# Optimization experiments

Hardware: AMD Instinct MI355X
Metric: run time of the kernel (lower is better)

## Reference

```python
import jax, jax.numpy as jnp
import numpy as np

N_NODES = 50000
N_EDGES = 800000
FEAT = 64
HID = 128
N_TYPES = 4
N_REL = 3
N_LAYERS = 2
LN_EPS = 1e-5


def setup_inputs() -> dict:
    key = jax.random.key(0)
    ks = jax.random.split(key, 20)
    inp = {
        "z": jax.random.randint(ks[0], (N_NODES,), 0, 100, dtype=jnp.int32),
        "node_type": jax.random.randint(ks[1], (N_NODES,), 0, N_TYPES, dtype=jnp.int32),
        "edge_index": jax.random.randint(ks[2], (2, N_EDGES), 0, N_NODES, dtype=jnp.int32),
        "edge_type": jax.random.randint(ks[3], (N_EDGES,), 0, N_REL, dtype=jnp.int32),
        # learned parameters
        "z_embed": jax.random.normal(ks[4], (100, FEAT), jnp.float32),
        "enc_w1": jax.random.normal(ks[5], (N_TYPES, FEAT, HID), jnp.float32) * 0.05,
        "enc_b1": jnp.zeros((N_TYPES, HID), jnp.float32),
        "enc_w2": jax.random.normal(ks[6], (N_TYPES, HID, HID), jnp.float32) * 0.05,
        "enc_b2": jnp.zeros((N_TYPES, HID), jnp.float32),
        "lin_w": jax.random.normal(ks[7], (N_LAYERS, HID, HID), jnp.float32) * 0.05,
        "lin_b": jnp.zeros((N_LAYERS, HID), jnp.float32),
        "rel_w": jax.random.normal(ks[8], (N_LAYERS, N_REL, HID, HID), jnp.float32) * 0.05,
        "ln_g": jnp.ones((N_LAYERS, HID), jnp.float32),
        "ln_b": jnp.zeros((N_LAYERS, HID), jnp.float32),
        "reg_w": jax.random.normal(ks[9], (HID, 1), jnp.float32) * 0.05,
        "reg_b": jnp.zeros((1,), jnp.float32),
    }
    return inp


def _layer_norm(x, g, b):
    mu = jnp.mean(x, axis=-1, keepdims=True)
    var = jnp.mean((x - mu) ** 2, axis=-1, keepdims=True)
    return (x - mu) * jax.lax.rsqrt(var + LN_EPS) * g + b


def reference(z, node_type, edge_index, edge_type, z_embed, enc_w1, enc_b1,
              enc_w2, enc_b2, lin_w, lin_b, rel_w, ln_g, ln_b, reg_w, reg_b):
    n = z.shape[0]
    # FeatureBuilder (site_ads=None path): atomic-number embedding lookup
    raw = z_embed[z]  # [N, FEAT]
    # TypeSpecificEncoder: run all 4 type MLPs, select per node by node_type
    h = jax.nn.relu(jnp.einsum('nd,tdh->nth', raw, enc_w1) + enc_b1)  # [N,T,H]
    enc_all = jnp.einsum('nth,tho->nto', h, enc_w2) + enc_b2           # [N,T,H]
    x = jnp.take_along_axis(enc_all, node_type[:, None, None].astype(jnp.int32), axis=1)[:, 0, :]

    src, dst = edge_index[0], edge_index[1]
    deg = jax.ops.segment_sum(jnp.ones((edge_type.shape[0],), x.dtype), dst, num_segments=n)
    deg = jnp.clip(deg, 1.0, None)[:, None]  # [N,1]

    for l in range(N_LAYERS):
        out = jnp.zeros_like(x)
        x_src = x[src]  # [E, H] gathered source features
        for r in range(N_REL):
            mask = (edge_type == r).astype(x.dtype)[:, None]
            msg = (x_src * mask) @ rel_w[l, r]  # [E, H]
            out = out + jax.ops.segment_sum(msg, dst, num_segments=n)
        out = out / deg
        x = _layer_norm(x @ lin_w[l] + lin_b[l] + out, ln_g[l], ln_b[l])

    pooled = jnp.mean(x, axis=0)  # mean pooling, mask = all ones
    return pooled @ reg_w + reg_b  # [1]
```

## Files before the change

kernel.cpp:

```cpp
#include <hip/hip_runtime.h>

#define N_NODES 50000
#define N_EDGES 800000
#define FEAT 64
#define HID 128
#define N_TYPES 4
#define N_REL 3
#define N_LAYERS 2
#define LN_EPS 1e-5f
#define NROWS 50016
#define NG32 1563
#define CAP 64
#define NBKT 196
#define CAP1 4608
#define EPB 4096
#define BINCAP 56
#define NCOMBO 400
#define WT_STRIDE 136

typedef __attribute__((ext_vector_type(8))) short bf16x8;
typedef __attribute__((ext_vector_type(16))) float f32x16;
typedef __attribute__((ext_vector_type(2))) float f32x2;

static __device__ inline unsigned short f2bf(float f) {
    unsigned int u = __float_as_uint(f);
    return (unsigned short)((u + 0x7fffu + ((u >> 16) & 1u)) >> 16);
}
static __device__ inline unsigned int packbf2(float lo, float hi) {
    return (unsigned int)f2bf(lo) | ((unsigned int)f2bf(hi) << 16);
}

static __device__ inline void acc8_fp8(float* a, uint2 w) {
    f32x2 d0 = __builtin_amdgcn_cvt_pk_f32_fp8((int)w.x, false);
    f32x2 d1 = __builtin_amdgcn_cvt_pk_f32_fp8((int)w.x, true);
    f32x2 d2 = __builtin_amdgcn_cvt_pk_f32_fp8((int)w.y, false);
    f32x2 d3 = __builtin_amdgcn_cvt_pk_f32_fp8((int)w.y, true);
    a[0] += d0[0]; a[1] += d0[1]; a[2] += d1[0]; a[3] += d1[1];
    a[4] += d2[0]; a[5] += d2[1]; a[6] += d3[0]; a[7] += d3[1];
}

__global__ __launch_bounds__(256) void build_tables_kernel(
    const int* __restrict__ src, const int* __restrict__ dst,
    const int* __restrict__ et, const int* __restrict__ z,
    const int* __restrict__ nt,
    const float* __restrict__ z_embed, const float* __restrict__ w1,
    const float* __restrict__ b1, const float* __restrict__ w2,
    const float* __restrict__ b2, const float* __restrict__ rel_w,
    const float* __restrict__ lin_w, const float* __restrict__ lin_b,
    unsigned short* __restrict__ combo, int* __restrict__ bcnt,
    int* __restrict__ bucket, unsigned int* __restrict__ ytab,
    float* __restrict__ lintab, unsigned short* __restrict__ wbuf,
    float* __restrict__ pooled) {
    __shared__ int lbin[NBKT * BINCAP];
    __shared__ int lcnt[NBKT];
    __shared__ int lbase[NBKT];
    __shared__ float h[HID];
    __shared__ float xrow[HID];
    __shared__ float tmp[HID];

    int b = blockIdx.x;
    if (b < NBKT) {
        int ci = b * 256 + threadIdx.x;
        if (ci < N_NODES) combo[ci] = (unsigned short)(z[ci] * 4 + nt[ci]);
        for (int i = threadIdx.x; i < NBKT; i += 256) lcnt[i] = 0;
        __syncthreads();
        int base = b * EPB;
#pragma unroll
        for (int i = 0; i < EPB / 256; ++i) {
            int e = base + i * 256 + threadIdx.x;
            if (e < N_EDGES) {
                int d = dst[e];
                int bk = d >> 8;
                int v = src[e] | (et[e] << 16) | ((d & 255) << 18);
                int pos = atomicAdd(&lcnt[bk], 1);
                if (pos < BINCAP) lbin[bk * BINCAP + pos] = v;
            }
        }
        __syncthreads();
        if (threadIdx.x < NBKT) {
            int c = min(lcnt[threadIdx.x], BINCAP);
            lcnt[threadIdx.x] = c;
            lbase[threadIdx.x] = atomicAdd(&bcnt[threadIdx.x], c);
        }
        __syncthreads();
        int wv = threadIdx.x >> 6, ln = threadIdx.x & 63;
        for (int bb = wv; bb < NBKT; bb += 4) {
            int c = lcnt[bb];
            if (ln < c) {
                int gp = lbase[bb] + ln;
                if (gp < CAP1) bucket[bb * CAP1 + gp] = lbin[bb * BINCAP + ln];
            }
        }
        return;
    }
    if (b >= NBKT + NCOMBO) {
        int pb = b - (NBKT + NCOMBO);
        if (pb == 0 && threadIdx.x < HID) pooled[threadIdx.x] = 0.0f;
        int idx = pb * 256 + threadIdx.x;
        int k = idx & 127;
        int col = (idx >> 7) & 127;
        int mat = idx >> 14;
        float w = (mat < 3) ? rel_w[(((size_t)(3 + mat)) * HID + k) * HID + col]
                            : lin_w[((size_t)(HID + k)) * HID + col];
        wbuf[(size_t)mat * HID * WT_STRIDE + col * WT_STRIDE + k] = f2bf(w);
        return;
    }
    int c = b - NBKT;
    int zi = c >> 2;
    int t = c & 3;
    int j = threadIdx.x;
    bool act = j < HID;
    if (act) {
        float acc = b1[t * HID + j];
#pragma unroll 8
        for (int k = 0; k < FEAT; ++k)
            acc = fmaf(z_embed[zi * FEAT + k], w1[((size_t)t * FEAT + k) * HID + j], acc);
        h[j] = fmaxf(acc, 0.0f);
    }
    __syncthreads();
    if (act) {
        float acc2 = b2[t * HID + j];
#pragma unroll 8
        for (int k = 0; k < HID; ++k)
            acc2 = fmaf(h[k], w2[(size_t)t * HID * HID + k * HID + j], acc2);
        xrow[j] = acc2;
    }
    __syncthreads();
#pragma unroll 1
    for (int r = 0; r < N_REL; ++r) {
        if (act) {
            float a = 0.f;
            const float* W = rel_w + (size_t)r * HID * HID;
#pragma unroll 8
            for (int k = 0; k < HID; ++k) a = fmaf(xrow[k], W[k * HID + j], a);
            tmp[j] = a;
        }
        __syncthreads();
        if (j < 32) {
            int w0 = __builtin_amdgcn_cvt_pk_fp8_f32(tmp[4 * j], tmp[4 * j + 1], 0, false);
            w0 = __builtin_amdgcn_cvt_pk_fp8_f32(tmp[4 * j + 2], tmp[4 * j + 3], w0, true);
            ytab[(r * NCOMBO + c) * 32 + j] = (unsigned)w0;
        }
        __syncthreads();
    }
    if (act) {
        float a = lin_b[j];
#pragma unroll 8
        for (int k = 0; k < HID; ++k) a = fmaf(xrow[k], lin_w[k * HID + j], a);
        lintab[c * HID + j] = a;
    }
}

__global__ __launch_bounds__(256) void build2_kernel(const int* __restrict__ bcnt,
                                                     const int* __restrict__ bucket,
                                                     const unsigned short* __restrict__ combo,
                                                     int* __restrict__ cnt3,
                                                     int* __restrict__ payload) {
    __shared__ int lcnt[256 * 3];
    for (int i = threadIdx.x; i < 768; i += 256) lcnt[i] = 0;
    __syncthreads();
    int b = blockIdx.x;
    int n0 = b << 8;
    int cb = min(bcnt[b], CAP1);
    const int* bk = bucket + b * CAP1;
    for (int i = threadIdx.x; i < cb; i += 256) {
        int v = bk[i];
        atomicAdd(&lcnt[((v >> 18) & 255) * 3 + ((v >> 16) & 3)], 1);
    }
    __syncthreads();
    int t = threadIdx.x;
    int c0 = min(lcnt[t * 3 + 0], CAP);
    int c1 = min(lcnt[t * 3 + 1], CAP - c0);
    int c2 = min(lcnt[t * 3 + 2], CAP - c0 - c1);
    __syncthreads();
    lcnt[t * 3 + 0] = 0;
    lcnt[t * 3 + 1] = c0;
    lcnt[t * 3 + 2] = c0 + c1;
    int node = n0 + t;
    if (node < N_NODES) cnt3[node] = c0 | (c1 << 8) | (c2 << 16);
    __syncthreads();
    for (int i = threadIdx.x; i < cb; i += 256) {
        int v = bk[i];
        int dl = (v >> 18) & 255;
        int r = (v >> 16) & 3;
        int sc = v & 0xffff;
        int pos = atomicAdd(&lcnt[dl * 3 + r], 1);
        if (pos < CAP)
            payload[((n0 + dl) << 6) + pos] = sc | ((int)combo[sc] << 18);
    }
}

__global__ __launch_bounds__(256) void gather_ln1_kernel(
    const int* __restrict__ cnt3, const int* __restrict__ payload,
    const uint2* __restrict__ ytab8, const float* __restrict__ lintab,
    const unsigned short* __restrict__ combo, const float* __restrict__ lng,
    const float* __restrict__ lnb, uint4* __restrict__ xb4,
    uint2* __restrict__ xf8) {
    int tid = blockIdx.x * 256 + threadIdx.x;
    int node = tid >> 4;
    int l16 = tid & 15;
    int c3 = cnt3[node];
    int c0 = c3 & 255, c1 = (c3 >> 8) & 255, c2 = (c3 >> 16) & 255;
    int tot = c0 + c1 + c2;
    float inv = 1.0f / (float)max(tot, 1);
    const int* pl = payload + (node << 6);
    float a[8] = {};
    int e = 0;
#pragma unroll 1
    for (int r = 0; r < 3; ++r) {
        int e1 = (r == 0) ? c0 : (r == 1) ? c0 + c1 : tot;
        int base = (r * NCOMBO) << 4;
        for (; e + 4 <= e1; e += 4) {
            int pA = pl[e], pB = pl[e + 1], pC = pl[e + 2], pD = pl[e + 3];
            uint2 vA = ytab8[base + ((pA >> 18) << 4) + l16];
            uint2 vB = ytab8[base + ((pB >> 18) << 4) + l16];
            uint2 vC = ytab8[base + ((pC >> 18) << 4) + l16];
            uint2 vD = ytab8[base + ((pD >> 18) << 4) + l16];
            acc8_fp8(a, vA);
            acc8_fp8(a, vB);
            acc8_fp8(a, vC);
            acc8_fp8(a, vD);
        }
        if (e + 2 <= e1) {
            int pA = pl[e], pB = pl[e + 1];
            uint2 vA = ytab8[base + ((pA >> 18) << 4) + l16];
            uint2 vB = ytab8[base + ((pB >> 18) << 4) + l16];
            acc8_fp8(a, vA);
            acc8_fp8(a, vB);
            e += 2;
        }
        if (e < e1) {
            int p = pl[e]; ++e;
            acc8_fp8(a, ytab8[base + ((p >> 18) << 4) + l16]);
        }
    }
    const float* lrow = lintab + (int)combo[node] * HID + l16 * 8;
    float v[8], s = 0.f, q = 0.f;
#pragma unroll
    for (int j = 0; j < 8; ++j) {
        v[j] = fmaf(a[j], inv, lrow[j]);
        s += v[j];
        q += v[j] * v[j];
    }
#pragma unroll
    for (int mk = 1; mk < 16; mk <<= 1) {
        s += __shfl_xor(s, mk);
        q += __shfl_xor(q, mk);
    }
    float mu = s * (1.0f / HID);
    float rstd = rsqrtf(q * (1.0f / HID) - mu * mu + LN_EPS);
    const float* g8 = lng + l16 * 8;
    const float* b8 = lnb + l16 * 8;
    float o[8];
#pragma unroll
    for (int j = 0; j < 8; ++j) o[j] = (v[j] - mu) * rstd * g8[j] + b8[j];
    uint4 w;
    w.x = packbf2(o[0], o[1]);
    w.y = packbf2(o[2], o[3]);
    w.z = packbf2(o[4], o[5]);
    w.w = packbf2(o[6], o[7]);
    xb4[(node << 4) + l16] = w;
    int lo = 0, hi = 0;
    lo = __builtin_amdgcn_cvt_pk_fp8_f32(o[0], o[1], lo, false);
    lo = __builtin_amdgcn_cvt_pk_fp8_f32(o[2], o[3], lo, true);
    hi = __builtin_amdgcn_cvt_pk_fp8_f32(o[4], o[5], hi, false);
    hi = __builtin_amdgcn_cvt_pk_fp8_f32(o[6], o[7], hi, true);
    xf8[(node << 4) + l16] = make_uint2((unsigned)lo, (unsigned)hi);
}

__global__ __launch_bounds__(256) void gather3_kernel(const int* __restrict__ cnt3,
                                                      const int* __restrict__ payload,
                                                      const uint2* __restrict__ xf8,
                                                      uint4* __restrict__ s0,
                                                      uint4* __restrict__ s1,
                                                      uint4* __restrict__ s2) {
    int tid = blockIdx.x * 256 + threadIdx.x;
    int node = tid >> 4;
    int l16 = tid & 15;
    int c3 = cnt3[node];
    int c0 = c3 & 255, c1 = (c3 >> 8) & 255, c2 = (c3 >> 16) & 255;
    int tot = c0 + c1 + c2;
    float inv = 1.0f / (float)max(tot, 1);
    const int* pl = payload + (node << 6);
    int o = node * 16 + l16;
    int e = 0;
#pragma unroll 1
    for (int r = 0; r < 3; ++r) {
        int e1 = (r == 0) ? c0 : (r == 1) ? c0 + c1 : tot;
        float a[8] = {};
        for (; e + 4 <= e1; e += 4) {
            int pA = pl[e], pB = pl[e + 1], pC = pl[e + 2], pD = pl[e + 3];
            uint2 vA = xf8[((pA & 0xffff) << 4) + l16];
            uint2 vB = xf8[((pB & 0xffff) << 4) + l16];
            uint2 vC = xf8[((pC & 0xffff) << 4) + l16];
            uint2 vD = xf8[((pD & 0xffff) << 4) + l16];
            acc8_fp8(a, vA);
            acc8_fp8(a, vB);
            acc8_fp8(a, vC);
            acc8_fp8(a, vD);
        }
        if (e + 2 <= e1) {
            int pA = pl[e], pB = pl[e + 1];
            uint2 vA = xf8[((pA & 0xffff) << 4) + l16];
            uint2 vB = xf8[((pB & 0xffff) << 4) + l16];
            acc8_fp8(a, vA);
            acc8_fp8(a, vB);
            e += 2;
        }
        if (e < e1) {
            int p = pl[e]; ++e;
            acc8_fp8(a, xf8[((p & 0xffff) << 4) + l16]);
        }
        uint4 w;
        w.x = packbf2(a[0] * inv, a[1] * inv);
        w.y = packbf2(a[2] * inv, a[3] * inv);
        w.z = packbf2(a[4] * inv, a[5] * inv);
        w.w = packbf2(a[6] * inv, a[7] * inv);
        if (r == 0) s0[o] = w;
        else if (r == 1) s1[o] = w;
        else s2[o] = w;
    }
}

__global__ __launch_bounds__(512) void fused_layer_kernel(
    const unsigned short* __restrict__ s0, const unsigned short* __restrict__ s1,
    const unsigned short* __restrict__ s2, const unsigned short* __restrict__ xb,
    const uint4* __restrict__ wbuf, const float* __restrict__ lb,
    const float* __restrict__ lng, const float* __restrict__ lnb,
    float* __restrict__ pooled, const float* __restrict__ reg_w,
    const float* __restrict__ reg_b, float* __restrict__ out,
    int* __restrict__ done) {
    __shared__ __align__(16) unsigned short Wt[4 * HID * WT_STRIDE];
    __shared__ float csh[3 * HID];
    __shared__ float pooled_sh[HID];
    __shared__ int lastFlag;

    if (threadIdx.x < HID) {
        pooled_sh[threadIdx.x] = 0.0f;
        csh[threadIdx.x] = lb[threadIdx.x];
        csh[HID + threadIdx.x] = lng[threadIdx.x];
        csh[2 * HID + threadIdx.x] = lnb[threadIdx.x];
    }
    uint4* wt4 = (uint4*)Wt;
#pragma unroll
    for (int i = 0; i < 17; ++i)
        wt4[i * 512 + threadIdx.x] = wbuf[i * 512 + threadIdx.x];
    __syncthreads();

    int wave = threadIdx.x >> 6;
    int lane = threadIdx.x & 63;
    int n32 = lane & 31;
    int hf = lane >> 5;

    float pacc[4] = {0.f, 0.f, 0.f, 0.f};

    for (int g = wave * gridDim.x + blockIdx.x; g < NG32; g += gridDim.x * 8) {
        int node0 = g * 32;
        f32x16 acc[4];
#pragma unroll
        for (int ct = 0; ct < 4; ++ct)
#pragma unroll
            for (int i = 0; i < 16; ++i) acc[ct][i] = 0.0f;

#pragma unroll 1
        for (int mat = 0; mat < 4; ++mat) {
            const unsigned short* asrc = (mat == 0) ? s0 : (mat == 1) ? s1
                                       : (mat == 2) ? s2 : xb;
            const unsigned short* arow = asrc + (size_t)(node0 + n32) * HID + hf * 8;
            const unsigned short* wm = Wt + mat * (HID * WT_STRIDE) + n32 * WT_STRIDE + hf * 8;
#pragma unroll 2
            for (int t = 0; t < 8; ++t) {
                bf16x8 a = *(const bf16x8*)(arow + t * 16);
#pragma unroll
                for (int ct = 0; ct < 4; ++ct) {
                    bf16x8 b = *(const bf16x8*)(wm + ct * 32 * WT_STRIDE + t * 16);
                    acc[ct] = __builtin_amdgcn_mfma_f32_32x32x16_bf16(a, b, acc[ct], 0, 0, 0);
                }
            }
        }
#pragma unroll
        for (int reg = 0; reg < 16; ++reg) {
            int row = node0 + (reg & 3) + 8 * (reg >> 2) + 4 * hf;
            float v[4];
            float s = 0.f, q = 0.f;
#pragma unroll
            for (int ct = 0; ct < 4; ++ct) {
                v[ct] = acc[ct][reg] + csh[ct * 32 + n32];
                s += v[ct];
                q += v[ct] * v[ct];
            }
#pragma unroll
            for (int mk = 1; mk < 32; mk <<= 1) {
                s += __shfl_xor(s, mk);
                q += __shfl_xor(q, mk);
            }
            float mu = s * (1.0f / HID);
            float rstd = rsqrtf(q * (1.0f / HID) - mu * mu + LN_EPS);
            if (row < N_NODES) {
#pragma unroll
                for (int ct = 0; ct < 4; ++ct) {
                    int col = ct * 32 + n32;
                    pacc[ct] += (v[ct] - mu) * rstd * csh[HID + col] + csh[2 * HID + col];
                }
            }
        }
    }

#pragma unroll
    for (int ct = 0; ct < 4; ++ct) {
        float t = pacc[ct] + __shfl_xor(pacc[ct], 32);
        if (hf == 0) atomicAdd(&pooled_sh[ct * 32 + n32], t);
    }
    __syncthreads();
    if (threadIdx.x < HID) atomicAdd(&pooled[threadIdx.x], pooled_sh[threadIdx.x]);

    __threadfence();
    __syncthreads();
    if (threadIdx.x == 0)
        lastFlag = (atomicAdd(done, 1) == (int)gridDim.x - 1);
    __syncthreads();
    if (lastFlag && threadIdx.x < 64) {
        int l = threadIdx.x;
        float s = atomicAdd(&pooled[l], 0.0f) * reg_w[l] +
                  atomicAdd(&pooled[64 + l], 0.0f) * reg_w[64 + l];
#pragma unroll
        for (int o = 32; o; o >>= 1) s += __shfl_down(s, o);
        if (l == 0) out[0] = s * (1.0f / N_NODES) + reg_b[0];
    }
}

extern "C" void kernel_launch(void* const* d_in, const int* in_sizes, int n_in,
                              void* d_out, int out_size, void* d_ws, size_t ws_size,
                              hipStream_t stream) {
    const int* z = (const int*)d_in[0];
    const int* nt = (const int*)d_in[1];
    const int* ei = (const int*)d_in[2];
    const int* et = (const int*)d_in[3];
    const float* z_embed = (const float*)d_in[4];
    const float* enc_w1 = (const float*)d_in[5];
    const float* enc_b1 = (const float*)d_in[6];
    const float* enc_w2 = (const float*)d_in[7];
    const float* enc_b2 = (const float*)d_in[8];
    const float* lin_w = (const float*)d_in[9];
    const float* lin_b = (const float*)d_in[10];
    const float* rel_w = (const float*)d_in[11];
    const float* ln_g = (const float*)d_in[12];
    const float* ln_b = (const float*)d_in[13];
    const float* reg_w = (const float*)d_in[14];
    const float* reg_b = (const float*)d_in[15];
    float* out = (float*)d_out;

    const size_t NHb = (size_t)NROWS * HID;
    char* p = (char*)d_ws;
    unsigned short* xb = (unsigned short*)p;    p += NHb * 2;
    unsigned short* s0 = (unsigned short*)p;    p += NHb * 2;
    unsigned short* s1 = (unsigned short*)p;    p += NHb * 2;
    unsigned short* s2 = (unsigned short*)p;    p += NHb * 2;
    uint2* xf8 = (uint2*)p;                     p += NHb;
    unsigned short* wbuf = (unsigned short*)p;  p += (size_t)4 * HID * WT_STRIDE * 2;
    unsigned int* ytab = (unsigned int*)p;      p += (size_t)N_REL * NCOMBO * HID;
    float* lintab = (float*)p;                  p += NCOMBO * HID * 4;
    unsigned short* combo = (unsigned short*)p; p += N_NODES * 2;
    float* pooled = (float*)p;                  p += HID * 4;
    int* cnt3 = (int*)p;                        p += N_NODES * 4;
    int* bcnt = (int*)p;                        p += NBKT * 4;
    int* done = (int*)p;                        p += 4;
    int* bucket = (int*)p;                      p += (size_t)NBKT * CAP1 * 4;
    int* payload = (int*)p;                     p += (size_t)N_NODES * CAP * 4;

    const int* src = ei;
    const int* dst = ei + N_EDGES;

    hipMemsetAsync(bcnt, 0, (NBKT + 1) * sizeof(int), stream);

    build_tables_kernel<<<NBKT + NCOMBO + 256, 256, 0, stream>>>(
        src, dst, et, z, nt, z_embed, enc_w1, enc_b1, enc_w2, enc_b2,
        rel_w, lin_w, lin_b, combo, bcnt, bucket, ytab, lintab, wbuf, pooled);

    build2_kernel<<<NBKT, 256, 0, stream>>>(bcnt, bucket, combo, cnt3, payload);

    gather_ln1_kernel<<<3125, 256, 0, stream>>>(cnt3, payload, (const uint2*)ytab, lintab,
                                                combo, ln_g, ln_b, (uint4*)xb, xf8);
    gather3_kernel<<<3125, 256, 0, stream>>>(cnt3, payload, xf8,
                                             (uint4*)s0, (uint4*)s1, (uint4*)s2);
    fused_layer_kernel<<<256, 512, 0, stream>>>(
        s0, s1, s2, xb, (const uint4*)wbuf, lin_b + HID, ln_g + HID, ln_b + HID,
        pooled, reg_w, reg_b, out, done);
}
```

Measured before the change: 233.6 us.

## Prefetch A-operand rows into double-buffered registers overlapping weight LDS fill

The fused layer kernel now issues global loads for the first matrix's A rows before the weight tile is staged into shared memory. It then double-buffers the remaining three matrices' rows in registers, so each load overlaps the MFMAs of the previous matrix. The grid-stride loop is replaced by a single group per wave, which assumes the grid has enough waves to cover all 32-node groups. The gain is hidden global-load latency, paid for with more vector registers and possibly lower occupancy.

```diff
diff --git a/kernel.cpp b/kernel.cpp
--- a/kernel.cpp
+++ b/kernel.cpp
@@ -335,6 +335,22 @@
     __shared__ float pooled_sh[HID];
     __shared__ int lastFlag;
 
+    int wave = threadIdx.x >> 6;
+    int lane = threadIdx.x & 63;
+    int n32 = lane & 31;
+    int hf = lane >> 5;
+
+    int g0 = wave * gridDim.x + blockIdx.x;
+    bool active = g0 < NG32;
+    size_t rofs = active ? ((size_t)(g0 * 32 + n32) * HID + hf * 8) : 0;
+
+    bf16x8 bufA[8], bufB[8];
+    {
+        const unsigned short* p0 = s0 + rofs;
+#pragma unroll
+        for (int t = 0; t < 8; ++t) bufA[t] = *(const bf16x8*)(p0 + t * 16);
+    }
+
     if (threadIdx.x < HID) {
         pooled_sh[threadIdx.x] = 0.0f;
         csh[threadIdx.x] = lb[threadIdx.x];
@@ -347,37 +363,48 @@
         wt4[i * 512 + threadIdx.x] = wbuf[i * 512 + threadIdx.x];
     __syncthreads();
 
-    int wave = threadIdx.x >> 6;
-    int lane = threadIdx.x & 63;
-    int n32 = lane & 31;
-    int hf = lane >> 5;
-
     float pacc[4] = {0.f, 0.f, 0.f, 0.f};
 
-    for (int g = wave * gridDim.x + blockIdx.x; g < NG32; g += gridDim.x * 8) {
-        int node0 = g * 32;
+    if (active) {
         f32x16 acc[4];
 #pragma unroll
         for (int ct = 0; ct < 4; ++ct)
 #pragma unroll
             for (int i = 0; i < 16; ++i) acc[ct][i] = 0.0f;
 
-#pragma unroll 1
-        for (int mat = 0; mat < 4; ++mat) {
-            const unsigned short* asrc = (mat == 0) ? s0 : (mat == 1) ? s1
-                                       : (mat == 2) ? s2 : xb;
-            const unsigned short* arow = asrc + (size_t)(node0 + n32) * HID + hf * 8;
-            const unsigned short* wm = Wt + mat * (HID * WT_STRIDE) + n32 * WT_STRIDE + hf * 8;
-#pragma unroll 2
-            for (int t = 0; t < 8; ++t) {
-                bf16x8 a = *(const bf16x8*)(arow + t * 16);
-#pragma unroll
-                for (int ct = 0; ct < 4; ++ct) {
-                    bf16x8 b = *(const bf16x8*)(wm + ct * 32 * WT_STRIDE + t * 16);
-                    acc[ct] = __builtin_amdgcn_mfma_f32_32x32x16_bf16(a, b, acc[ct], 0, 0, 0);
-                }
-            }
-        }
+        const unsigned short* wbase = Wt + n32 * WT_STRIDE + hf * 8;
+
+#define DOMAT(buf, m)                                                          \
+        {                                                                      \
+            const unsigned short* wm = wbase + (m) * (HID * WT_STRIDE);        \
+            _Pragma("unroll")                                                  \
+            for (int t = 0; t < 8; ++t) {                                      \
+                _Pragma("unroll")                                              \
+                for (int ct = 0; ct < 4; ++ct) {                               \
+                    bf16x8 bfr = *(const bf16x8*)(wm + ct * 32 * WT_STRIDE + t * 16); \
+                    acc[ct] = __builtin_amdgcn_mfma_f32_32x32x16_bf16(         \
+                        buf[t], bfr, acc[ct], 0, 0, 0);                        \
+                }                                                              \
+            }                                                                  \
+        }
+#define LDMAT(buf, srcp)                                                       \
+        {                                                                      \
+            const unsigned short* _p = (srcp) + rofs;                          \
+            _Pragma("unroll")                                                  \
+            for (int t = 0; t < 8; ++t) buf[t] = *(const bf16x8*)(_p + t * 16);\
+        }
+
+        LDMAT(bufB, s1);
+        DOMAT(bufA, 0);
+        LDMAT(bufA, s2);
+        DOMAT(bufB, 1);
+        LDMAT(bufB, xb);
+        DOMAT(bufA, 2);
+        DOMAT(bufB, 3);
+#undef DOMAT
+#undef LDMAT
+
+        int node0 = g0 * 32;
 #pragma unroll
         for (int reg = 0; reg < 16; ++reg) {
             int row = node0 + (reg & 3) + 8 * (reg >> 2) + 4 * hf;
```

Result: no change. 232.7 us (-0.4%).
